# Performance work log

Hardware: AMD Instinct MI355X
Metric: run time of the kernel (lower is better)

The kernel has to match this reference:

```python
import jax, jax.numpy as jnp
import numpy as np

B, L, D_MODEL, D_STATE, D_MAMBA, DT_RANK = 2, 1024, 1024, 16, 2048, 64
K_CONV = 4


def setup_inputs() -> dict:
    key = jax.random.key(0)
    ks = jax.random.split(key, 10)
    x = jax.random.normal(ks[0], (B, L, D_MODEL), dtype=jnp.float32)
    s_in = 1.0 / np.sqrt(D_MODEL)
    s_xm = 1.0 / np.sqrt(D_MAMBA)
    s_dt = 1.0 / np.sqrt(DT_RANK)
    W_in = jax.random.normal(ks[1], (D_MODEL, 2 * D_MAMBA), dtype=jnp.float32) * s_in
    conv_w = jax.random.normal(ks[2], (K_CONV, 1, D_MAMBA), dtype=jnp.float32) * 0.5  # depthwise kernel (W, I=1, O)
    conv_b = jnp.zeros((D_MAMBA,), dtype=jnp.float32)
    A_log = jax.random.uniform(ks[3], (D_MAMBA, D_STATE), dtype=jnp.float32, minval=-3.0, maxval=1.0)
    D = jnp.ones((D_MAMBA,), dtype=jnp.float32)
    W_x = jax.random.normal(ks[4], (D_MAMBA, DT_RANK + 2 * D_STATE), dtype=jnp.float32) * s_xm
    W_dt = jax.random.normal(ks[5], (DT_RANK, D_MAMBA), dtype=jnp.float32) * s_dt
    b_dt = jnp.zeros((D_MAMBA,), dtype=jnp.float32)
    W_out = jax.random.normal(ks[6], (D_MAMBA, D_MODEL), dtype=jnp.float32) * s_xm
    return {"x": x, "W_in": W_in, "conv_w": conv_w, "conv_b": conv_b,
            "A_log": A_log, "D": D, "W_x": W_x, "W_dt": W_dt, "b_dt": b_dt, "W_out": W_out}


def _silu(v):
    return v * jax.nn.sigmoid(v)


def reference(x, W_in, conv_w, conv_b, A_log, D, W_x, W_dt, b_dt, W_out):
    # in_proj and split
    xz = x @ W_in                                   # [B,L,2*dm]
    x_m, z = jnp.split(xz, 2, axis=-1)              # [B,L,dm] each
    # depthwise conv1d, TF 'same' padding for k=4 -> (left=1, right=2)
    x_m = jax.lax.conv_general_dilated(
        x_m, conv_w, window_strides=(1,), padding=[(1, 2)],
        dimension_numbers=("NWC", "WIO", "NWC"), feature_group_count=D_MAMBA) + conv_b
    x_m = _silu(x_m)
    # data-dependent SSM params
    x_dbl = x_m @ W_x                               # [B,L,dt_rank+2*ds]
    dt_low, Bc, Cc = jnp.split(x_dbl, [DT_RANK, DT_RANK + D_STATE], axis=-1)
    dt = jax.nn.softplus(dt_low @ W_dt + b_dt)      # [B,L,dm]
    A = -jnp.exp(A_log)                             # [dm,ds]
    dA = jnp.exp(dt[..., None] * A[None, None])     # [B,L,dm,ds]
    dB = dt[..., None] * Bc[:, :, None, :]          # [B,L,dm,ds]
    u = x_m[..., None]                              # [B,L,dm,1]
    # sequential selective scan over L
    dA_T = jnp.transpose(dA, (1, 0, 2, 3))
    dB_T = jnp.transpose(dB, (1, 0, 2, 3))
    u_T = jnp.transpose(u, (1, 0, 2, 3))

    def step(state, inp):
        da_t, db_t, u_t = inp
        s = da_t * state + db_t * u_t               # [B,dm,ds]
        return s, s

    init = jnp.zeros((x.shape[0], D_MAMBA, D_STATE), dtype=x.dtype)
    _, states = jax.lax.scan(step, init, (dA_T, dB_T, u_T))  # [L,B,dm,ds]
    states = jnp.transpose(states, (1, 0, 2, 3))    # [B,L,dm,ds]
    y = jnp.einsum("blms,bls->blm", states, Cc)     # [B,L,dm]
    y = y + x_m * D
    y = y * _silu(z)
    return y @ W_out                                # [B,L,d_model]
```

## Files before the change

kernel.cpp:

```cpp
#include <hip/hip_runtime.h>
#include <hip/hip_bf16.h>
#include <math.h>

#define BATCH 2
#define LSEQ 1024
#define DMODEL 1024
#define DSTATE 16
#define DMAMBA 2048
#define DTRANK 64
#define NTOK (BATCH * LSEQ)
#define NCHUNK 16
#define CLEN (LSEQ / NCHUNK)
#define NLANE (BATCH * DMAMBA * DSTATE)

typedef __attribute__((ext_vector_type(8))) short short8;
typedef __attribute__((ext_vector_type(4))) float f32x4;

static __device__ __forceinline__ unsigned short f2bf(float f) {
    union { float f; unsigned u; } v; v.f = f;
    unsigned r = v.u + 0x7FFF + ((v.u >> 16) & 1);
    return (unsigned short)(r >> 16);
}

__global__ __launch_bounds__(256) void cvt_bf16_kernel(
    const float* __restrict__ in, unsigned short* __restrict__ out, int n8)
{
    int i = blockIdx.x * 256 + threadIdx.x;
    if (i >= n8) return;
    const float4* p = (const float4*)(in + (size_t)i * 8);
    float4 a = p[0], b = p[1];
    unsigned short t[8];
    t[0]=f2bf(a.x); t[1]=f2bf(a.y); t[2]=f2bf(a.z); t[3]=f2bf(a.w);
    t[4]=f2bf(b.x); t[5]=f2bf(b.y); t[6]=f2bf(b.z); t[7]=f2bf(b.w);
    *(short8*)(out + (size_t)i * 8) = *(short8*)t;
}

__global__ __launch_bounds__(256) void cvt_dtl_kernel(
    const float* __restrict__ xdbl128, unsigned short* __restrict__ dtlb)
{
    int i = blockIdx.x * 256 + threadIdx.x;
    int r = i >> 3, c8 = (i & 7) * 8;
    const float* src = xdbl128 + (size_t)r * 128 + c8;
    unsigned short t[8];
    #pragma unroll
    for (int j = 0; j < 8; ++j) t[j] = f2bf(src[j]);
    *(short8*)(dtlb + (size_t)r * 64 + c8) = *(short8*)t;
}

__global__ __launch_bounds__(256) void transpose_bf16_kernel(
    const float* __restrict__ W, unsigned short* __restrict__ Wt, int K, int N)
{
    __shared__ unsigned short tile[32][33];
    int k0 = blockIdx.y * 32, n0 = blockIdx.x * 32;
    int tx = threadIdx.x & 31, ty = threadIdx.x >> 5;
    #pragma unroll
    for (int i = 0; i < 32; i += 8) {
        unsigned short v = 0;
        if (n0 + tx < N) v = f2bf(W[(size_t)(k0 + ty + i) * N + n0 + tx]);
        tile[ty + i][tx] = v;
    }
    __syncthreads();
    #pragma unroll
    for (int i = 0; i < 32; i += 8)
        Wt[(size_t)(n0 + ty + i) * K + k0 + tx] = tile[tx][ty + i];
}

template <int ACT>
__global__ __launch_bounds__(256) void gemm_mfma(
    const unsigned short* __restrict__ A, int lda,
    const unsigned short* __restrict__ Bt,
    const float* __restrict__ bias,
    float* __restrict__ C, int ldc,
    int K)
{
    __shared__ __attribute__((aligned(16))) unsigned short As[128][40];
    __shared__ __attribute__((aligned(16))) unsigned short Bs[128][40];
    int tid = threadIdx.x;
    int wave = tid >> 6, lane = tid & 63;
    int wr = wave >> 1, wc = wave & 1;
    int m0 = blockIdx.y * 128, n0 = blockIdx.x * 128;
    int srow = tid >> 1, skof = (tid & 1) * 16;
    int fr = lane & 15, fk = (lane >> 4) * 8;

    f32x4 acc[4][4] = {};

    for (int k0 = 0; k0 < K; k0 += 32) {
        {
            const unsigned short* asrc = &A[(size_t)(m0 + srow) * lda + k0 + skof];
            *(short8*)&As[srow][skof]     = *(const short8*)asrc;
            *(short8*)&As[srow][skof + 8] = *(const short8*)(asrc + 8);
            const unsigned short* bsrc = &Bt[(size_t)(n0 + srow) * K + k0 + skof];
            *(short8*)&Bs[srow][skof]     = *(const short8*)bsrc;
            *(short8*)&Bs[srow][skof + 8] = *(const short8*)(bsrc + 8);
        }
        __syncthreads();
        short8 afr[4], bfr[4];
        #pragma unroll
        for (int i = 0; i < 4; ++i) afr[i] = *(const short8*)&As[wr * 64 + i * 16 + fr][fk];
        #pragma unroll
        for (int j = 0; j < 4; ++j) bfr[j] = *(const short8*)&Bs[wc * 64 + j * 16 + fr][fk];
        #pragma unroll
        for (int i = 0; i < 4; ++i)
            #pragma unroll
            for (int j = 0; j < 4; ++j)
                acc[i][j] = __builtin_amdgcn_mfma_f32_16x16x32_bf16(afr[i], bfr[j], acc[i][j], 0, 0, 0);
        __syncthreads();
    }

    #pragma unroll
    for (int i = 0; i < 4; ++i) {
        int rbase = m0 + wr * 64 + i * 16 + 4 * (lane >> 4);
        #pragma unroll
        for (int j = 0; j < 4; ++j) {
            int col = n0 + wc * 64 + j * 16 + (lane & 15);
            #pragma unroll
            for (int r = 0; r < 4; ++r) {
                float v = acc[i][j][r];
                if (bias) v += bias[col];
                if (ACT == 1) v = (v > 20.f) ? v : log1pf(expf(v));
                C[(size_t)(rbase + r) * ldc + col] = v;
            }
        }
    }
}

__global__ __launch_bounds__(256) void conv_silu_kernel(
    const float* __restrict__ xz,
    const float* __restrict__ cw,
    const float* __restrict__ cb,
    float* __restrict__ xm,
    unsigned short* __restrict__ xmb)
{
    int idx = blockIdx.x * 256 + threadIdx.x;
    if (idx >= NTOK * DMAMBA) return;
    int c = idx & (DMAMBA - 1);
    int t = idx >> 11;
    int b = t >> 10;
    int l = t & (LSEQ - 1);
    float acc = cb[c];
    #pragma unroll
    for (int k = 0; k < 4; ++k) {
        int li = l - 1 + k;
        if (li >= 0 && li < LSEQ)
            acc = fmaf(xz[(size_t)(b * LSEQ + li) * (2 * DMAMBA) + c], cw[k * DMAMBA + c], acc);
    }
    float s = acc / (1.f + expf(-acc));
    xm[(size_t)t * DMAMBA + c] = s;
    xmb[(size_t)t * DMAMBA + c] = f2bf(s);
}

__global__ __launch_bounds__(256) void scanA_kernel(
    const float* __restrict__ dt,
    const float* __restrict__ xm,
    const float* __restrict__ xdbl,
    const float* __restrict__ A_log,
    float* __restrict__ aprod_buf,
    float* __restrict__ send_buf)
{
    int tid = threadIdx.x;
    int s = tid & 15;
    int g = blockIdx.x * 16 + (tid >> 4);
    int c = blockIdx.y;
    int m = g & (DMAMBA - 1);
    int b = g >> 11;
    float Ams = -expf(A_log[m * DSTATE + s]);
    float ap = 1.f, se = 0.f;
    int row0 = b * LSEQ + c * CLEN;
    for (int l = 0; l < CLEN; l += 4) {
        float dtv[4], uu[4], Bv[4];
        #pragma unroll
        for (int q = 0; q < 4; ++q) {
            int row = row0 + l + q;
            dtv[q] = dt[(size_t)row * DMAMBA + m];
            uu[q]  = xm[(size_t)row * DMAMBA + m];
            Bv[q]  = xdbl[(size_t)row * 128 + DTRANK + s];
        }
        #pragma unroll
        for (int q = 0; q < 4; ++q) {
            float dA = __expf(dtv[q] * Ams);
            se = fmaf(dA, se, dtv[q] * Bv[q] * uu[q]);
            ap *= dA;
        }
    }
    int li = blockIdx.x * 256 + tid;
    aprod_buf[(size_t)c * NLANE + li] = ap;
    send_buf[(size_t)c * NLANE + li] = se;
}

__global__ __launch_bounds__(256) void scanB_kernel(
    const float* __restrict__ aprod_buf,
    const float* __restrict__ send_buf,
    float* __restrict__ sin_buf)
{
    int li = blockIdx.x * 256 + threadIdx.x;
    float sp = 0.f;
    #pragma unroll
    for (int c = 0; c < NCHUNK; ++c) {
        float a = aprod_buf[(size_t)c * NLANE + li];
        float e = send_buf[(size_t)c * NLANE + li];
        sin_buf[(size_t)c * NLANE + li] = sp;
        sp = e + a * sp;
    }
}

__global__ __launch_bounds__(256) void scanC_kernel(
    const float* __restrict__ dt,
    const float* __restrict__ xm,
    const float* __restrict__ xdbl,
    const float* __restrict__ A_log,
    const float* __restrict__ Dv,
    const float* __restrict__ sin_buf,
    const float* __restrict__ zbuf,
    unsigned short* __restrict__ ybuf)
{
    int tid = threadIdx.x;
    int s = tid & 15;
    int g = blockIdx.x * 16 + (tid >> 4);
    int c = blockIdx.y;
    int m = g & (DMAMBA - 1);
    int b = g >> 11;
    float Ams = -expf(A_log[m * DSTATE + s]);
    float Dm = Dv[m];
    int li = blockIdx.x * 256 + tid;
    float state = sin_buf[(size_t)c * NLANE + li];
    int row0 = b * LSEQ + c * CLEN;
    for (int l = 0; l < CLEN; l += 4) {
        float dtv[4], uu[4], Bv[4], Cv[4];
        #pragma unroll
        for (int q = 0; q < 4; ++q) {
            int row = row0 + l + q;
            dtv[q] = dt[(size_t)row * DMAMBA + m];
            uu[q]  = xm[(size_t)row * DMAMBA + m];
            Bv[q]  = xdbl[(size_t)row * 128 + DTRANK + s];
            Cv[q]  = xdbl[(size_t)row * 128 + DTRANK + DSTATE + s];
        }
        #pragma unroll
        for (int q = 0; q < 4; ++q) {
            int row = row0 + l + q;
            float dA = __expf(dtv[q] * Ams);
            state = fmaf(dA, state, dtv[q] * Bv[q] * uu[q]);
            float p = state * Cv[q];
            p += __shfl_xor(p, 1);
            p += __shfl_xor(p, 2);
            p += __shfl_xor(p, 4);
            p += __shfl_xor(p, 8);
            if (s == 0) {
                float zv = zbuf[(size_t)row * (2 * DMAMBA) + m];
                float yv = (p + uu[q] * Dm) * (zv / (1.f + expf(-zv)));
                ybuf[(size_t)row * (4 * DMAMBA) + m] = f2bf(yv);
            }
        }
    }
}

extern "C" void kernel_launch(void* const* d_in, const int* in_sizes, int n_in,
                              void* d_out, int out_size, void* d_ws, size_t ws_size,
                              hipStream_t stream) {
    const float* x      = (const float*)d_in[0];
    const float* W_in   = (const float*)d_in[1];
    const float* conv_w = (const float*)d_in[2];
    const float* conv_b = (const float*)d_in[3];
    const float* A_log  = (const float*)d_in[4];
    const float* Dv     = (const float*)d_in[5];
    const float* W_x    = (const float*)d_in[6];
    const float* W_dt   = (const float*)d_in[7];
    const float* b_dt   = (const float*)d_in[8];
    const float* W_out  = (const float*)d_in[9];
    float* out = (float*)d_out;

    const size_t M1 = 1048576;
    float* ws      = (float*)d_ws;
    float* xz      = ws;
    float* xm      = xz + 8 * M1;
    float* dtb     = xm + 4 * M1;
    float* xdbl128 = dtb + 4 * M1;
    float* scanR   = xdbl128 + 2048 * 128;
    float* aprod   = scanR;
    float* send    = scanR + M1;
    float* sinb    = scanR + 2 * M1;
    unsigned short* xb   = (unsigned short*)scanR;
    unsigned short* WinT = (unsigned short*)(scanR + M1);
    unsigned short* xmb  = (unsigned short*)scanR;
    float* tail    = scanR + 3 * M1;
    unsigned short* WoutT = (unsigned short*)tail;
    unsigned short* WxT   = (unsigned short*)(tail + M1);
    unsigned short* WdtT  = WxT + 128 * 2048;
    unsigned short* dtlb  = WdtT + 2048 * 64;
    unsigned short* yb    = (unsigned short*)xz;

    dim3 blk(256);

    cvt_bf16_kernel<<<dim3(NTOK * DMODEL / 8 / 256), blk, 0, stream>>>(x, xb, NTOK * DMODEL / 8);
    transpose_bf16_kernel<<<dim3(4096 / 32, 1024 / 32), blk, 0, stream>>>(W_in, WinT, DMODEL, 2 * DMAMBA);

    gemm_mfma<0><<<dim3(32, 16), blk, 0, stream>>>(xb, DMODEL, WinT, nullptr, xz, 2 * DMAMBA, DMODEL);

    conv_silu_kernel<<<dim3(NTOK * DMAMBA / 256), blk, 0, stream>>>(xz, conv_w, conv_b, xm, xmb);

    transpose_bf16_kernel<<<dim3(1024 / 32, 2048 / 32), blk, 0, stream>>>(W_out, WoutT, DMAMBA, DMODEL);
    transpose_bf16_kernel<<<dim3(128 / 32, 2048 / 32), blk, 0, stream>>>(W_x, WxT, DMAMBA, 96);
    transpose_bf16_kernel<<<dim3(2048 / 32, 64 / 32), blk, 0, stream>>>(W_dt, WdtT, DTRANK, DMAMBA);

    gemm_mfma<0><<<dim3(1, 16), blk, 0, stream>>>(xmb, DMAMBA, WxT, nullptr, xdbl128, 128, DMAMBA);

    cvt_dtl_kernel<<<dim3(64), blk, 0, stream>>>(xdbl128, dtlb);

    gemm_mfma<1><<<dim3(16, 16), blk, 0, stream>>>(dtlb, DTRANK, WdtT, b_dt, dtb, DMAMBA, DTRANK);

    scanA_kernel<<<dim3(256, NCHUNK), blk, 0, stream>>>(dtb, xm, xdbl128, A_log, aprod, send);
    scanB_kernel<<<dim3(NLANE / 256), blk, 0, stream>>>(aprod, send, sinb);
    scanC_kernel<<<dim3(256, NCHUNK), blk, 0, stream>>>(dtb, xm, xdbl128, A_log, Dv, sinb, xz + DMAMBA, yb);

    gemm_mfma<0><<<dim3(8, 16), blk, 0, stream>>>(yb, 4 * DMAMBA, WoutT, nullptr, out, DMODEL, DMAMBA);
}
```

Baseline: 440.5 us.

## Fuse dt projection and softplus into scan kernels, drop dt GEMM

Removes the separate dt_low conversion, W_dt transpose and dt GEMM kernels. Each scanA/scanC block now computes its own 64x16 tile of dt (dt_low @ W_dt + bias, softplus) in fp32 in shared memory before scanning. This avoids writing and twice re-reading a 16 MB fp32 dt buffer and saves three launches. The cost is that the small matmul is computed twice (once in scanA, once in scanC), plus extra shared memory and syncs per block.

```diff
diff --git a/kernel.cpp b/kernel.cpp
--- a/kernel.cpp
+++ b/kernel.cpp
@@ -35,18 +35,6 @@
     *(short8*)(out + (size_t)i * 8) = *(short8*)t;
 }
 
-__global__ __launch_bounds__(256) void cvt_dtl_kernel(
-    const float* __restrict__ xdbl128, unsigned short* __restrict__ dtlb)
-{
-    int i = blockIdx.x * 256 + threadIdx.x;
-    int r = i >> 3, c8 = (i & 7) * 8;
-    const float* src = xdbl128 + (size_t)r * 128 + c8;
-    unsigned short t[8];
-    #pragma unroll
-    for (int j = 0; j < 8; ++j) t[j] = f2bf(src[j]);
-    *(short8*)(dtlb + (size_t)r * 64 + c8) = *(short8*)t;
-}
-
 __global__ __launch_bounds__(256) void transpose_bf16_kernel(
     const float* __restrict__ W, unsigned short* __restrict__ Wt, int K, int N)
 {
@@ -149,29 +137,79 @@
     xmb[(size_t)t * DMAMBA + c] = f2bf(s);
 }
 
+__device__ __forceinline__ void compute_dt_tile(
+    const float* __restrict__ xdbl, const float* __restrict__ W_dt,
+    const float* __restrict__ b_dt, int row0, int m0, int tid,
+    float (*dtl)[65], float (*wdt)[16], float (*dts)[17])
+{
+    {
+        int r = tid >> 4;
+        int c4 = (tid & 15) * 4;
+        #pragma unroll
+        for (int q = 0; q < 4; ++q) {
+            int row = q * 16 + r;
+            float4 v = *(const float4*)&xdbl[(size_t)(row0 + row) * 128 + c4];
+            dtl[row][c4] = v.x; dtl[row][c4 + 1] = v.y;
+            dtl[row][c4 + 2] = v.z; dtl[row][c4 + 3] = v.w;
+        }
+        int k = tid >> 4, mi = tid & 15;
+        #pragma unroll
+        for (int q = 0; q < 4; ++q)
+            wdt[q * 16 + k][mi] = W_dt[(size_t)(q * 16 + k) * DMAMBA + m0 + mi];
+    }
+    __syncthreads();
+    {
+        int rA = (tid >> 3) * 2;
+        int miA = (tid & 7) * 2;
+        float acc00 = b_dt[m0 + miA],     acc01 = b_dt[m0 + miA + 1];
+        float acc10 = acc00,              acc11 = acc01;
+        #pragma unroll
+        for (int k = 0; k < 64; ++k) {
+            float a0 = dtl[rA][k], a1 = dtl[rA + 1][k];
+            float w0 = wdt[k][miA], w1 = wdt[k][miA + 1];
+            acc00 = fmaf(a0, w0, acc00); acc01 = fmaf(a0, w1, acc01);
+            acc10 = fmaf(a1, w0, acc10); acc11 = fmaf(a1, w1, acc11);
+        }
+        dts[rA][miA]         = (acc00 > 20.f) ? acc00 : log1pf(__expf(acc00));
+        dts[rA][miA + 1]     = (acc01 > 20.f) ? acc01 : log1pf(__expf(acc01));
+        dts[rA + 1][miA]     = (acc10 > 20.f) ? acc10 : log1pf(__expf(acc10));
+        dts[rA + 1][miA + 1] = (acc11 > 20.f) ? acc11 : log1pf(__expf(acc11));
+    }
+    __syncthreads();
+}
+
 __global__ __launch_bounds__(256) void scanA_kernel(
-    const float* __restrict__ dt,
     const float* __restrict__ xm,
     const float* __restrict__ xdbl,
+    const float* __restrict__ W_dt,
+    const float* __restrict__ b_dt,
     const float* __restrict__ A_log,
     float* __restrict__ aprod_buf,
     float* __restrict__ send_buf)
 {
+    __shared__ float dtl[CLEN][65];
+    __shared__ float wdt[64][16];
+    __shared__ float dts[CLEN][17];
     int tid = threadIdx.x;
+    int c = blockIdx.y;
+    int g0 = blockIdx.x * 16;
+    int m0 = g0 & (DMAMBA - 1);
+    int b  = g0 >> 11;
+    int row0 = b * LSEQ + c * CLEN;
+
+    compute_dt_tile(xdbl, W_dt, b_dt, row0, m0, tid, dtl, wdt, dts);
+
     int s = tid & 15;
-    int g = blockIdx.x * 16 + (tid >> 4);
-    int c = blockIdx.y;
-    int m = g & (DMAMBA - 1);
-    int b = g >> 11;
+    int mloc = tid >> 4;
+    int m = m0 + mloc;
     float Ams = -expf(A_log[m * DSTATE + s]);
     float ap = 1.f, se = 0.f;
-    int row0 = b * LSEQ + c * CLEN;
     for (int l = 0; l < CLEN; l += 4) {
         float dtv[4], uu[4], Bv[4];
         #pragma unroll
         for (int q = 0; q < 4; ++q) {
             int row = row0 + l + q;
-            dtv[q] = dt[(size_t)row * DMAMBA + m];
+            dtv[q] = dts[l + q][mloc];
             uu[q]  = xm[(size_t)row * DMAMBA + m];
             Bv[q]  = xdbl[(size_t)row * 128 + DTRANK + s];
         }
@@ -204,32 +242,41 @@
 }
 
 __global__ __launch_bounds__(256) void scanC_kernel(
-    const float* __restrict__ dt,
     const float* __restrict__ xm,
     const float* __restrict__ xdbl,
+    const float* __restrict__ W_dt,
+    const float* __restrict__ b_dt,
     const float* __restrict__ A_log,
     const float* __restrict__ Dv,
     const float* __restrict__ sin_buf,
     const float* __restrict__ zbuf,
     unsigned short* __restrict__ ybuf)
 {
+    __shared__ float dtl[CLEN][65];
+    __shared__ float wdt[64][16];
+    __shared__ float dts[CLEN][17];
     int tid = threadIdx.x;
+    int c = blockIdx.y;
+    int g0 = blockIdx.x * 16;
+    int m0 = g0 & (DMAMBA - 1);
+    int b  = g0 >> 11;
+    int row0 = b * LSEQ + c * CLEN;
+
+    compute_dt_tile(xdbl, W_dt, b_dt, row0, m0, tid, dtl, wdt, dts);
+
     int s = tid & 15;
-    int g = blockIdx.x * 16 + (tid >> 4);
-    int c = blockIdx.y;
-    int m = g & (DMAMBA - 1);
-    int b = g >> 11;
+    int mloc = tid >> 4;
+    int m = m0 + mloc;
     float Ams = -expf(A_log[m * DSTATE + s]);
     float Dm = Dv[m];
     int li = blockIdx.x * 256 + tid;
     float state = sin_buf[(size_t)c * NLANE + li];
-    int row0 = b * LSEQ + c * CLEN;
     for (int l = 0; l < CLEN; l += 4) {
         float dtv[4], uu[4], Bv[4], Cv[4];
         #pragma unroll
         for (int q = 0; q < 4; ++q) {
             int row = row0 + l + q;
-            dtv[q] = dt[(size_t)row * DMAMBA + m];
+            dtv[q] = dts[l + q][mloc];
             uu[q]  = xm[(size_t)row * DMAMBA + m];
             Bv[q]  = xdbl[(size_t)row * 128 + DTRANK + s];
             Cv[q]  = xdbl[(size_t)row * 128 + DTRANK + DSTATE + s];
@@ -284,8 +331,6 @@
     float* tail    = scanR + 3 * M1;
     unsigned short* WoutT = (unsigned short*)tail;
     unsigned short* WxT   = (unsigned short*)(tail + M1);
-    unsigned short* WdtT  = WxT + 128 * 2048;
-    unsigned short* dtlb  = WdtT + 2048 * 64;
     unsigned short* yb    = (unsigned short*)xz;
 
     dim3 blk(256);
@@ -299,17 +344,12 @@
 
     transpose_bf16_kernel<<<dim3(1024 / 32, 2048 / 32), blk, 0, stream>>>(W_out, WoutT, DMAMBA, DMODEL);
     transpose_bf16_kernel<<<dim3(128 / 32, 2048 / 32), blk, 0, stream>>>(W_x, WxT, DMAMBA, 96);
-    transpose_bf16_kernel<<<dim3(2048 / 32, 64 / 32), blk, 0, stream>>>(W_dt, WdtT, DTRANK, DMAMBA);
 
     gemm_mfma<0><<<dim3(1, 16), blk, 0, stream>>>(xmb, DMAMBA, WxT, nullptr, xdbl128, 128, DMAMBA);
 
-    cvt_dtl_kernel<<<dim3(64), blk, 0, stream>>>(xdbl128, dtlb);
-
-    gemm_mfma<1><<<dim3(16, 16), blk, 0, stream>>>(dtlb, DTRANK, WdtT, b_dt, dtb, DMAMBA, DTRANK);
-
-    scanA_kernel<<<dim3(256, NCHUNK), blk, 0, stream>>>(dtb, xm, xdbl128, A_log, aprod, send);
+    scanA_kernel<<<dim3(256, NCHUNK), blk, 0, stream>>>(xm, xdbl128, W_dt, b_dt, A_log, aprod, send);
     scanB_kernel<<<dim3(NLANE / 256), blk, 0, stream>>>(aprod, send, sinb);
-    scanC_kernel<<<dim3(256, NCHUNK), blk, 0, stream>>>(dtb, xm, xdbl128, A_log, Dv, sinb, xz + DMAMBA, yb);
+    scanC_kernel<<<dim3(256, NCHUNK), blk, 0, stream>>>(xm, xdbl128, W_dt, b_dt, A_log, Dv, sinb, xz + DMAMBA, yb);
 
     gemm_mfma<0><<<dim3(8, 16), blk, 0, stream>>>(yb, 4 * DMAMBA, WoutT, nullptr, out, DMODEL, DMAMBA);
 }
```

New measurement: 974.9 us. +121.3%, slower.
